# Optimization experiments

Hardware: AMD Instinct MI355X
Metric: run time of the kernel (lower is better)

## Reference

```python
import jax, jax.numpy as jnp
import numpy as np

EPS = 1e-7  # keras.backend.epsilon()
ROUTINGS = 3
N_IN, D_IN = 2048, 16
CAPS_N, CAPS_DIM = 64, 32
BATCH = 32


def squash(x, axis=-1):
    s2 = jnp.sum(jnp.square(x), axis=axis, keepdims=True) + EPS
    return (jnp.sqrt(s2) / (1.0 + s2)) * x


def setup_inputs() -> dict:
    key = jax.random.key(0)
    kx, kw = jax.random.split(key)
    x = jax.random.normal(kx, (BATCH, N_IN, D_IN), dtype=jnp.float32)
    # glorot_uniform for W: fan_in = caps_dim_in, fan_out = caps_dim_out (per matmul tile)
    limit = np.sqrt(6.0 / (D_IN + CAPS_DIM))
    W = jax.random.uniform(kw, (N_IN, CAPS_N, CAPS_DIM, D_IN), minval=-limit, maxval=limit, dtype=jnp.float32)
    return {"x": x, "W": W}


def reference(x, W):
    # caps_predicted (u_hat): W[i,k] @ x[b,i] -> [B, n_in, caps_n, caps_dim]
    u_hat = jnp.einsum('ikdl,bil->bikd', W, x)
    # routing logits, broadcast over batch like the original [1, n_in, caps_n, 1, 1]
    b = jnp.zeros((1, N_IN, CAPS_N), dtype=x.dtype)
    v = None
    for r in range(ROUTINGS):
        c = jax.nn.softmax(b, axis=2)                      # [*, n_in, caps_n]
        s = jnp.sum(c[..., None] * u_hat, axis=1)          # [B, caps_n, caps_dim]
        v = squash(s, axis=-1)                             # [B, caps_n, caps_dim]
        if r < ROUTINGS - 1:
            # agreement = u_hat^T . v  -> [B, n_in, caps_n]
            agreement = jnp.einsum('bikd,bkd->bik', u_hat, v)
            b = b + agreement
    return v
```

## Files before the change

### kernel.cpp

```cpp
#include <hip/hip_runtime.h>
#include <hip/hip_fp16.h>

#define BB 32
#define NI 2048
#define NK 64
#define ND 32
#define NL 16
#define KD (NK*ND)
#define CHUNK 32
#define NCH (NI/CHUNK)
#define EPSF 1e-7f

struct __align__(16) H8 { __half2 h[4]; };
struct __align__(8)  H4 { __half2 h[2]; };

__global__ __launch_bounds__(512) void k_uhat(const float* __restrict__ x,
                                              const float* __restrict__ W,
                                              __half* __restrict__ uhat) {
  const int i = blockIdx.x;
  const int t = threadIdx.x;
  __shared__ float xs[BB * NL];
  {
    const int b = t >> 4, l = t & 15;
    xs[t] = x[((size_t)b * NI + i) * NL + l];
  }
  __syncthreads();
  float w[4][NL];
  const float* Wp = W + (size_t)i * KD * NL + (size_t)t * 4 * NL;
  #pragma unroll
  for (int c = 0; c < 4; ++c)
    #pragma unroll
    for (int q = 0; q < 4; ++q)
      *(float4*)&w[c][q * 4] = *(const float4*)(Wp + c * NL + q * 4);
  __half* up = uhat + (size_t)i * KD + (size_t)t * 4;
  for (int b = 0; b < BB; ++b) {
    float a0 = 0.f, a1 = 0.f, a2 = 0.f, a3 = 0.f;
    #pragma unroll
    for (int l = 0; l < NL; ++l) {
      const float xv = xs[b * NL + l];
      a0 += w[0][l] * xv; a1 += w[1][l] * xv;
      a2 += w[2][l] * xv; a3 += w[3][l] * xv;
    }
    H4 o;
    o.h[0] = __floats2half2_rn(a0, a1);
    o.h[1] = __floats2half2_rn(a2, a3);
    *(H4*)(up + (size_t)b * NI * KD) = o;
  }
}

__global__ __launch_bounds__(256) void k_round0(const __half* __restrict__ uhat,
                                                float* __restrict__ partial) {
  const int ch = blockIdx.x, b = blockIdx.y, t = threadIdx.x;
  float acc[8];
  #pragma unroll
  for (int j = 0; j < 8; ++j) acc[j] = 0.f;
  const __half* up = uhat + ((size_t)b * NI + (size_t)ch * CHUNK) * KD + t * 8;
  for (int il = 0; il < CHUNK; ++il) {
    H8 u = *(const H8*)(up + (size_t)il * KD);
    #pragma unroll
    for (int j = 0; j < 4; ++j) {
      float2 f = __half22float2(u.h[j]);
      acc[2 * j]     += f.x;
      acc[2 * j + 1] += f.y;
    }
  }
  float* pp = partial + ((size_t)b * NCH + ch) * KD + t * 8;
  #pragma unroll
  for (int j = 0; j < 8; ++j) pp[j] = acc[j] * (1.f / 64.f);
}

template <int ROUND>
__global__ __launch_bounds__(256) void k_route(const __half* __restrict__ uhat,
                                               const float* __restrict__ vin,
                                               const float* __restrict__ bin,
                                               float* __restrict__ bout,
                                               float* __restrict__ partial) {
  const int ch = blockIdx.x, b = blockIdx.y, t = threadIdx.x;
  const int k = t >> 2;
  const int lane = t & 63, w = t >> 6;
  float vr[8];
  {
    const float* vp = vin + (size_t)b * KD + t * 8;
    #pragma unroll
    for (int j = 0; j < 8; ++j) vr[j] = vp[j];
  }
  float sacc[8];
  #pragma unroll
  for (int j = 0; j < 8; ++j) sacc[j] = 0.f;
  __shared__ float smax[4], ssum[4];
  const __half* up = uhat + ((size_t)b * NI + (size_t)ch * CHUNK) * KD + t * 8;
  const float* bip = bin + ((size_t)b * NI + (size_t)ch * CHUNK) * NK + k;
  float* bop = (ROUND == 1) ? bout + ((size_t)b * NI + (size_t)ch * CHUNK) * NK + k : nullptr;
  for (int il = 0; il < CHUNK; ++il) {
    H8 u = *(const H8*)(up + (size_t)il * KD);
    float uf[8];
    #pragma unroll
    for (int j = 0; j < 4; ++j) {
      float2 f = __half22float2(u.h[j]);
      uf[2 * j] = f.x; uf[2 * j + 1] = f.y;
    }
    float p = 0.f;
    #pragma unroll
    for (int j = 0; j < 8; ++j) p += uf[j] * vr[j];
    p += __shfl_xor(p, 1);
    p += __shfl_xor(p, 2);
    float bn = p;
    if (ROUND == 2) bn += bip[il * NK];
    if (ROUND == 1) { if ((t & 3) == 0) bop[il * NK] = p; }
    float m = bn;
    m = fmaxf(m, __shfl_xor(m, 4));
    m = fmaxf(m, __shfl_xor(m, 8));
    m = fmaxf(m, __shfl_xor(m, 16));
    m = fmaxf(m, __shfl_xor(m, 32));
    if (lane == 0) smax[w] = m;
    __syncthreads();
    m = fmaxf(fmaxf(smax[0], smax[1]), fmaxf(smax[2], smax[3]));
    const float e = __expf(bn - m);
    float s = e;
    s += __shfl_xor(s, 4);
    s += __shfl_xor(s, 8);
    s += __shfl_xor(s, 16);
    s += __shfl_xor(s, 32);
    if (lane == 0) ssum[w] = s;
    __syncthreads();
    s = ssum[0] + ssum[1] + ssum[2] + ssum[3];
    const float c = e / s;
    #pragma unroll
    for (int j = 0; j < 8; ++j) sacc[j] += c * uf[j];
  }
  float* pp = partial + ((size_t)b * NCH + ch) * KD + t * 8;
  #pragma unroll
  for (int j = 0; j < 8; ++j) pp[j] = sacc[j];
}

__global__ __launch_bounds__(256) void k_reduce(const float* __restrict__ partial,
                                                float* __restrict__ vout) {
  const int g = blockIdx.x, b = blockIdx.y, t = threadIdx.x;
  const int cell = g * 256 + t;
  float s = 0.f;
  const float* pp = partial + (size_t)b * NCH * KD + cell;
  for (int ch = 0; ch < NCH; ++ch) s += pp[(size_t)ch * KD];
  float sq = s * s;
  sq += __shfl_xor(sq, 1);
  sq += __shfl_xor(sq, 2);
  sq += __shfl_xor(sq, 4);
  sq += __shfl_xor(sq, 8);
  sq += __shfl_xor(sq, 16);
  sq += EPSF;
  const float scale = sqrtf(sq) / (1.f + sq);
  vout[(size_t)b * KD + cell] = s * scale;
}

extern "C" void kernel_launch(void* const* d_in, const int* in_sizes, int n_in,
                              void* d_out, int out_size, void* d_ws, size_t ws_size,
                              hipStream_t stream) {
  const float* x = (const float*)d_in[0];
  const float* W = (const float*)d_in[1];
  float* out = (float*)d_out;
  char* ws = (char*)d_ws;
  __half* uhat  = (__half*)ws;
  float* blog   = (float*)(ws + 268435456ull);
  float* part   = (float*)(ws + 268435456ull + 16777216ull);
  float* v      = (float*)(ws + 268435456ull + 2ull * 16777216);

  k_uhat<<<NI, 512, 0, stream>>>(x, W, uhat);
  k_round0<<<dim3(NCH, BB), 256, 0, stream>>>(uhat, part);
  k_reduce<<<dim3(8, BB), 256, 0, stream>>>(part, v);
  k_route<1><<<dim3(NCH, BB), 256, 0, stream>>>(uhat, v, v, blog, part);
  k_reduce<<<dim3(8, BB), 256, 0, stream>>>(part, v);
  k_route<2><<<dim3(NCH, BB), 256, 0, stream>>>(uhat, v, blog, nullptr, part);
  k_reduce<<<dim3(8, BB), 256, 0, stream>>>(part, out);
}
```

Baseline: 303.6 us.

## Recompute u_hat per routing round from fp16 W instead of materializing it

Drops the 256MB fp16 u_hat buffer and its three full reads. The first kernel converts W to a packed fp16 copy and fuses round 0's sum into the same pass. Each routing round then recomputes u_hat on the fly with fdot2, computes agreement and softmax per input tile in shared memory, and accumulates weighted partial sums. Logits are no longer stored: the reduce kernel adds the previous v, so the round-2 agreement uses u·(v1+v2). Partials are stored in fp16. This trades memory traffic for extra compute and lower-precision partial sums.

```diff
diff --git a/kernel.cpp b/kernel.cpp
--- a/kernel.cpp
+++ b/kernel.cpp
@@ -7,148 +7,221 @@
 #define ND 32
 #define NL 16
 #define KD (NK*ND)
-#define CHUNK 32
-#define NCH (NI/CHUNK)
+#define IT 8
+#define NT (NI/IT)
 #define EPSF 1e-7f
 
-struct __align__(16) H8 { __half2 h[4]; };
-struct __align__(8)  H4 { __half2 h[2]; };
-
-__global__ __launch_bounds__(512) void k_uhat(const float* __restrict__ x,
-                                              const float* __restrict__ W,
-                                              __half* __restrict__ uhat) {
-  const int i = blockIdx.x;
-  const int t = threadIdx.x;
-  __shared__ float xs[BB * NL];
+typedef _Float16 h2 __attribute__((ext_vector_type(2)));
+
+union U4H8 { uint4 u; h2 h[4]; };
+union UH2  { unsigned u; h2 h; };
+
+static __device__ __forceinline__ float dot2f(h2 a, h2 b, float c) {
+#if __has_builtin(__builtin_amdgcn_fdot2)
+  return __builtin_amdgcn_fdot2(a, b, c, false);
+#else
+  return c + (float)a[0] * (float)b[0] + (float)a[1] * (float)b[1];
+#endif
+}
+
+static __device__ __forceinline__ h2 pack2(float x, float y) {
+  h2 r; r[0] = (_Float16)x; r[1] = (_Float16)y; return r;
+}
+
+static __device__ __forceinline__ void stage_x(const float* __restrict__ x,
+                                               h2 (*xs)[BB][8], int i0, int t) {
+  for (int q = t; q < IT * BB * 8; q += 512) {
+    const int l2 = q & 7, b = (q >> 3) & 31, ii = q >> 8;
+    const float2 f = *(const float2*)&x[((size_t)b * NI + (i0 + ii)) * NL + 2 * l2];
+    xs[ii][b][l2] = pack2(f.x, f.y);
+  }
+}
+
+__global__ __launch_bounds__(512, 2) void k_conv(const float* __restrict__ x,
+                                                 const float* __restrict__ W,
+                                                 uint4* __restrict__ Whs,
+                                                 __half* __restrict__ part) {
+  const int blk = blockIdx.x, t = threadIdx.x;
+  const int i0 = blk * IT;
+  __shared__ h2 xs[IT][BB][8];
+  stage_x(x, xs, i0, t);
+  __syncthreads();
+
+  float sacc[4][BB];
+  #pragma unroll
+  for (int c = 0; c < 4; ++c)
+    #pragma unroll
+    for (int b = 0; b < BB; ++b) sacc[c][b] = 0.f;
+
+  for (int ii = 0; ii < IT; ++ii) {
+    const float* Wp = W + ((size_t)(i0 + ii) * KD + 4 * t) * NL;
+    h2 wh[4][8];
+    #pragma unroll
+    for (int c = 0; c < 4; ++c) {
+      const float4 f0 = *(const float4*)(Wp + c * NL + 0);
+      const float4 f1 = *(const float4*)(Wp + c * NL + 4);
+      const float4 f2 = *(const float4*)(Wp + c * NL + 8);
+      const float4 f3 = *(const float4*)(Wp + c * NL + 12);
+      wh[c][0] = pack2(f0.x, f0.y); wh[c][1] = pack2(f0.z, f0.w);
+      wh[c][2] = pack2(f1.x, f1.y); wh[c][3] = pack2(f1.z, f1.w);
+      wh[c][4] = pack2(f2.x, f2.y); wh[c][5] = pack2(f2.z, f2.w);
+      wh[c][6] = pack2(f3.x, f3.y); wh[c][7] = pack2(f3.z, f3.w);
+      U4H8 a, b2;
+      a.h[0] = wh[c][0]; a.h[1] = wh[c][1]; a.h[2] = wh[c][2]; a.h[3] = wh[c][3];
+      b2.h[0] = wh[c][4]; b2.h[1] = wh[c][5]; b2.h[2] = wh[c][6]; b2.h[3] = wh[c][7];
+      Whs[((size_t)(i0 + ii) * 8 + 2 * c) * 512 + t]     = a.u;
+      Whs[((size_t)(i0 + ii) * 8 + 2 * c + 1) * 512 + t] = b2.u;
+    }
+    #pragma unroll
+    for (int b = 0; b < BB; ++b) {
+      U4H8 ux0, ux1;
+      ux0.u = *(const uint4*)&xs[ii][b][0];
+      ux1.u = *(const uint4*)&xs[ii][b][4];
+      float u0 = 0.f, u1 = 0.f, u2 = 0.f, u3 = 0.f;
+      #pragma unroll
+      for (int j = 0; j < 4; ++j) {
+        u0 = dot2f(wh[0][j], ux0.h[j], u0); u0 = dot2f(wh[0][4 + j], ux1.h[j], u0);
+        u1 = dot2f(wh[1][j], ux0.h[j], u1); u1 = dot2f(wh[1][4 + j], ux1.h[j], u1);
+        u2 = dot2f(wh[2][j], ux0.h[j], u2); u2 = dot2f(wh[2][4 + j], ux1.h[j], u2);
+        u3 = dot2f(wh[3][j], ux0.h[j], u3); u3 = dot2f(wh[3][4 + j], ux1.h[j], u3);
+      }
+      sacc[0][b] += u0; sacc[1][b] += u1; sacc[2][b] += u2; sacc[3][b] += u3;
+    }
+  }
+  #pragma unroll
+  for (int b = 0; b < BB; ++b) {
+    UH2 p0, p1;
+    p0.h = pack2(sacc[0][b] * (1.f / 64.f), sacc[1][b] * (1.f / 64.f));
+    p1.h = pack2(sacc[2][b] * (1.f / 64.f), sacc[3][b] * (1.f / 64.f));
+    *(uint2*)&part[((size_t)b * NT + blk) * KD + 4 * t] = make_uint2(p0.u, p1.u);
+  }
+}
+
+__global__ __launch_bounds__(512, 2) void k_route(const float* __restrict__ x,
+                                                  const uint4* __restrict__ Whs,
+                                                  const float* __restrict__ vin,
+                                                  __half* __restrict__ part) {
+  const int blk = blockIdx.x, t = threadIdx.x;
+  const int i0 = blk * IT;
+  const int k = t >> 3;
+  const int lane = t & 63, wv = t >> 6;
+  __shared__ h2 xs[IT][BB][8];
+  __shared__ h2 uS[BB][KD / 2];
+  __shared__ float smc[BB][NK];
+  stage_x(x, xs, i0, t);
+  __syncthreads();
+
+  float sacc[4][BB];
+  #pragma unroll
+  for (int c = 0; c < 4; ++c)
+    #pragma unroll
+    for (int b = 0; b < BB; ++b) sacc[c][b] = 0.f;
+
+  h2 wh[4][8];
   {
-    const int b = t >> 4, l = t & 15;
-    xs[t] = x[((size_t)b * NI + i) * NL + l];
-  }
-  __syncthreads();
-  float w[4][NL];
-  const float* Wp = W + (size_t)i * KD * NL + (size_t)t * 4 * NL;
-  #pragma unroll
-  for (int c = 0; c < 4; ++c)
-    #pragma unroll
-    for (int q = 0; q < 4; ++q)
-      *(float4*)&w[c][q * 4] = *(const float4*)(Wp + c * NL + q * 4);
-  __half* up = uhat + (size_t)i * KD + (size_t)t * 4;
+    #pragma unroll
+    for (int q = 0; q < 8; ++q) {
+      U4H8 r; r.u = Whs[((size_t)i0 * 8 + q) * 512 + t];
+      wh[q >> 1][(q & 1) * 4 + 0] = r.h[0]; wh[q >> 1][(q & 1) * 4 + 1] = r.h[1];
+      wh[q >> 1][(q & 1) * 4 + 2] = r.h[2]; wh[q >> 1][(q & 1) * 4 + 3] = r.h[3];
+    }
+  }
+
+  for (int ii = 0; ii < IT; ++ii) {
+    for (int b = 0; b < BB; ++b) {
+      U4H8 ux0, ux1;
+      ux0.u = *(const uint4*)&xs[ii][b][0];
+      ux1.u = *(const uint4*)&xs[ii][b][4];
+      float u0 = 0.f, u1 = 0.f, u2 = 0.f, u3 = 0.f;
+      #pragma unroll
+      for (int j = 0; j < 4; ++j) {
+        u0 = dot2f(wh[0][j], ux0.h[j], u0); u0 = dot2f(wh[0][4 + j], ux1.h[j], u0);
+        u1 = dot2f(wh[1][j], ux0.h[j], u1); u1 = dot2f(wh[1][4 + j], ux1.h[j], u1);
+        u2 = dot2f(wh[2][j], ux0.h[j], u2); u2 = dot2f(wh[2][4 + j], ux1.h[j], u2);
+        u3 = dot2f(wh[3][j], ux0.h[j], u3); u3 = dot2f(wh[3][4 + j], ux1.h[j], u3);
+      }
+      const float4 vv = *(const float4*)&vin[(size_t)b * KD + 4 * t];
+      float ag = u0 * vv.x + u1 * vv.y + u2 * vv.z + u3 * vv.w;
+      ag += __shfl_xor(ag, 1); ag += __shfl_xor(ag, 2); ag += __shfl_xor(ag, 4);
+      UH2 a0, a1; a0.h = pack2(u0, u1); a1.h = pack2(u2, u3);
+      *(uint2*)&uS[b][2 * t] = make_uint2(a0.u, a1.u);
+      if ((t & 7) == 0) smc[b][k] = ag;
+    }
+    uint4 pf[8];
+    if (ii + 1 < IT) {
+      #pragma unroll
+      for (int q = 0; q < 8; ++q)
+        pf[q] = Whs[((size_t)(i0 + ii + 1) * 8 + q) * 512 + t];
+    }
+    __syncthreads();
+    #pragma unroll
+    for (int j = 0; j < 4; ++j) {
+      const int b = wv * 4 + j;
+      const float lg = smc[b][lane];
+      float m = lg;
+      m = fmaxf(m, __shfl_xor(m, 1));  m = fmaxf(m, __shfl_xor(m, 2));
+      m = fmaxf(m, __shfl_xor(m, 4));  m = fmaxf(m, __shfl_xor(m, 8));
+      m = fmaxf(m, __shfl_xor(m, 16)); m = fmaxf(m, __shfl_xor(m, 32));
+      const float e = __expf(lg - m);
+      float s = e;
+      s += __shfl_xor(s, 1);  s += __shfl_xor(s, 2);  s += __shfl_xor(s, 4);
+      s += __shfl_xor(s, 8);  s += __shfl_xor(s, 16); s += __shfl_xor(s, 32);
+      smc[b][lane] = e / s;
+    }
+    __syncthreads();
+    #pragma unroll
+    for (int b = 0; b < BB; ++b) {
+      const float c_ = smc[b][k];
+      const uint2 up = *(const uint2*)&uS[b][2 * t];
+      UH2 w0, w1; w0.u = up.x; w1.u = up.y;
+      sacc[0][b] += c_ * (float)w0.h[0]; sacc[1][b] += c_ * (float)w0.h[1];
+      sacc[2][b] += c_ * (float)w1.h[0]; sacc[3][b] += c_ * (float)w1.h[1];
+    }
+    __syncthreads();
+    if (ii + 1 < IT) {
+      #pragma unroll
+      for (int q = 0; q < 8; ++q) {
+        U4H8 r; r.u = pf[q];
+        wh[q >> 1][(q & 1) * 4 + 0] = r.h[0]; wh[q >> 1][(q & 1) * 4 + 1] = r.h[1];
+        wh[q >> 1][(q & 1) * 4 + 2] = r.h[2]; wh[q >> 1][(q & 1) * 4 + 3] = r.h[3];
+      }
+    }
+  }
+  #pragma unroll
   for (int b = 0; b < BB; ++b) {
-    float a0 = 0.f, a1 = 0.f, a2 = 0.f, a3 = 0.f;
-    #pragma unroll
-    for (int l = 0; l < NL; ++l) {
-      const float xv = xs[b * NL + l];
-      a0 += w[0][l] * xv; a1 += w[1][l] * xv;
-      a2 += w[2][l] * xv; a3 += w[3][l] * xv;
-    }
-    H4 o;
-    o.h[0] = __floats2half2_rn(a0, a1);
-    o.h[1] = __floats2half2_rn(a2, a3);
-    *(H4*)(up + (size_t)b * NI * KD) = o;
-  }
-}
-
-__global__ __launch_bounds__(256) void k_round0(const __half* __restrict__ uhat,
-                                                float* __restrict__ partial) {
-  const int ch = blockIdx.x, b = blockIdx.y, t = threadIdx.x;
-  float acc[8];
-  #pragma unroll
-  for (int j = 0; j < 8; ++j) acc[j] = 0.f;
-  const __half* up = uhat + ((size_t)b * NI + (size_t)ch * CHUNK) * KD + t * 8;
-  for (int il = 0; il < CHUNK; ++il) {
-    H8 u = *(const H8*)(up + (size_t)il * KD);
-    #pragma unroll
-    for (int j = 0; j < 4; ++j) {
-      float2 f = __half22float2(u.h[j]);
-      acc[2 * j]     += f.x;
-      acc[2 * j + 1] += f.y;
-    }
-  }
-  float* pp = partial + ((size_t)b * NCH + ch) * KD + t * 8;
-  #pragma unroll
-  for (int j = 0; j < 8; ++j) pp[j] = acc[j] * (1.f / 64.f);
-}
-
-template <int ROUND>
-__global__ __launch_bounds__(256) void k_route(const __half* __restrict__ uhat,
-                                               const float* __restrict__ vin,
-                                               const float* __restrict__ bin,
-                                               float* __restrict__ bout,
-                                               float* __restrict__ partial) {
-  const int ch = blockIdx.x, b = blockIdx.y, t = threadIdx.x;
-  const int k = t >> 2;
-  const int lane = t & 63, w = t >> 6;
-  float vr[8];
-  {
-    const float* vp = vin + (size_t)b * KD + t * 8;
-    #pragma unroll
-    for (int j = 0; j < 8; ++j) vr[j] = vp[j];
-  }
-  float sacc[8];
-  #pragma unroll
-  for (int j = 0; j < 8; ++j) sacc[j] = 0.f;
-  __shared__ float smax[4], ssum[4];
-  const __half* up = uhat + ((size_t)b * NI + (size_t)ch * CHUNK) * KD + t * 8;
-  const float* bip = bin + ((size_t)b * NI + (size_t)ch * CHUNK) * NK + k;
-  float* bop = (ROUND == 1) ? bout + ((size_t)b * NI + (size_t)ch * CHUNK) * NK + k : nullptr;
-  for (int il = 0; il < CHUNK; ++il) {
-    H8 u = *(const H8*)(up + (size_t)il * KD);
-    float uf[8];
-    #pragma unroll
-    for (int j = 0; j < 4; ++j) {
-      float2 f = __half22float2(u.h[j]);
-      uf[2 * j] = f.x; uf[2 * j + 1] = f.y;
-    }
-    float p = 0.f;
-    #pragma unroll
-    for (int j = 0; j < 8; ++j) p += uf[j] * vr[j];
-    p += __shfl_xor(p, 1);
-    p += __shfl_xor(p, 2);
-    float bn = p;
-    if (ROUND == 2) bn += bip[il * NK];
-    if (ROUND == 1) { if ((t & 3) == 0) bop[il * NK] = p; }
-    float m = bn;
-    m = fmaxf(m, __shfl_xor(m, 4));
-    m = fmaxf(m, __shfl_xor(m, 8));
-    m = fmaxf(m, __shfl_xor(m, 16));
-    m = fmaxf(m, __shfl_xor(m, 32));
-    if (lane == 0) smax[w] = m;
-    __syncthreads();
-    m = fmaxf(fmaxf(smax[0], smax[1]), fmaxf(smax[2], smax[3]));
-    const float e = __expf(bn - m);
-    float s = e;
-    s += __shfl_xor(s, 4);
-    s += __shfl_xor(s, 8);
-    s += __shfl_xor(s, 16);
-    s += __shfl_xor(s, 32);
-    if (lane == 0) ssum[w] = s;
-    __syncthreads();
-    s = ssum[0] + ssum[1] + ssum[2] + ssum[3];
-    const float c = e / s;
-    #pragma unroll
-    for (int j = 0; j < 8; ++j) sacc[j] += c * uf[j];
-  }
-  float* pp = partial + ((size_t)b * NCH + ch) * KD + t * 8;
-  #pragma unroll
-  for (int j = 0; j < 8; ++j) pp[j] = sacc[j];
-}
-
-__global__ __launch_bounds__(256) void k_reduce(const float* __restrict__ partial,
+    UH2 p0, p1;
+    p0.h = pack2(sacc[0][b], sacc[1][b]);
+    p1.h = pack2(sacc[2][b], sacc[3][b]);
+    *(uint2*)&part[((size_t)b * NT + blk) * KD + 4 * t] = make_uint2(p0.u, p1.u);
+  }
+}
+
+__global__ __launch_bounds__(256) void k_reduce(const __half* __restrict__ part,
+                                                const float* __restrict__ vprev,
                                                 float* __restrict__ vout) {
   const int g = blockIdx.x, b = blockIdx.y, t = threadIdx.x;
-  const int cell = g * 256 + t;
-  float s = 0.f;
-  const float* pp = partial + (size_t)b * NCH * KD + cell;
-  for (int ch = 0; ch < NCH; ++ch) s += pp[(size_t)ch * KD];
-  float sq = s * s;
-  sq += __shfl_xor(sq, 1);
-  sq += __shfl_xor(sq, 2);
-  sq += __shfl_xor(sq, 4);
-  sq += __shfl_xor(sq, 8);
-  sq += __shfl_xor(sq, 16);
+  const int p = g * 256 + t;
+  const h2* pp = (const h2*)part;
+  const size_t base = (size_t)b * NT * (KD / 2) + p;
+  float sa0 = 0.f, sa1 = 0.f, sb0 = 0.f, sb1 = 0.f;
+  for (int ch = 0; ch < NT; ch += 2) {
+    const h2 va = pp[base + (size_t)ch * (KD / 2)];
+    const h2 vb = pp[base + (size_t)(ch + 1) * (KD / 2)];
+    sa0 += (float)va[0]; sa1 += (float)va[1];
+    sb0 += (float)vb[0]; sb1 += (float)vb[1];
+  }
+  const float s0 = sa0 + sb0, s1 = sa1 + sb1;
+  float sq = s0 * s0 + s1 * s1;
+  sq += __shfl_xor(sq, 1); sq += __shfl_xor(sq, 2);
+  sq += __shfl_xor(sq, 4); sq += __shfl_xor(sq, 8);
   sq += EPSF;
-  const float scale = sqrtf(sq) / (1.f + sq);
-  vout[(size_t)b * KD + cell] = s * scale;
+  const float sc = sqrtf(sq) / (1.f + sq);
+  float r0 = s0 * sc, r1 = s1 * sc;
+  if (vprev != nullptr) {
+    r0 += vprev[(size_t)b * KD + 2 * p];
+    r1 += vprev[(size_t)b * KD + 2 * p + 1];
+  }
+  *(float2*)&vout[(size_t)b * KD + 2 * p] = make_float2(r0, r1);
 }
 
 extern "C" void kernel_launch(void* const* d_in, const int* in_sizes, int n_in,
@@ -158,16 +231,15 @@
   const float* W = (const float*)d_in[1];
   float* out = (float*)d_out;
   char* ws = (char*)d_ws;
-  __half* uhat  = (__half*)ws;
-  float* blog   = (float*)(ws + 268435456ull);
-  float* part   = (float*)(ws + 268435456ull + 16777216ull);
-  float* v      = (float*)(ws + 268435456ull + 2ull * 16777216);
-
-  k_uhat<<<NI, 512, 0, stream>>>(x, W, uhat);
-  k_round0<<<dim3(NCH, BB), 256, 0, stream>>>(uhat, part);
-  k_reduce<<<dim3(8, BB), 256, 0, stream>>>(part, v);
-  k_route<1><<<dim3(NCH, BB), 256, 0, stream>>>(uhat, v, v, blog, part);
-  k_reduce<<<dim3(8, BB), 256, 0, stream>>>(part, v);
-  k_route<2><<<dim3(NCH, BB), 256, 0, stream>>>(uhat, v, blog, nullptr, part);
-  k_reduce<<<dim3(8, BB), 256, 0, stream>>>(part, out);
-}
+  uint4*  Whs  = (uint4*)ws;
+  __half* part = (__half*)(ws + 134217728ull);
+  float*  vA   = (float*)(ws + 134217728ull + 33554432ull);
+  float*  vB   = vA + (size_t)BB * KD;
+
+  k_conv<<<NT, 512, 0, stream>>>(x, W, Whs, part);
+  k_reduce<<<dim3(4, BB), 256, 0, stream>>>(part, nullptr, vA);
+  k_route<<<NT, 512, 0, stream>>>(x, Whs, vA, part);
+  k_reduce<<<dim3(4, BB), 256, 0, stream>>>(part, vA, vB);
+  k_route<<<NT, 512, 0, stream>>>(x, Whs, vB, part);
+  k_reduce<<<dim3(4, BB), 256, 0, stream>>>(part, nullptr, out);
+}
```

Measured after the change: 494.9 us. +63.0%, slower.
